# Optimization experiments

Measured on AMD Instinct MI355X. Metric: run time of the kernel, lower is better.

Reference implementation:

```python
import jax, jax.numpy as jnp
import numpy as np

DIM = 128
IND_DIM = 5
HEADS = 4
DIM_HEAD = 32
HIDDEN = HEADS * DIM_HEAD  # 128
SCALE = DIM_HEAD ** -0.5


def setup_inputs() -> dict:
    key = jax.random.key(0)
    ks = jax.random.split(key, 6)
    b, n = 1, 512
    x = jax.random.normal(ks[0], (b, DIM, n), dtype=jnp.float32)
    indicator = jax.random.normal(ks[1], (b, IND_DIM, n, n), dtype=jnp.float32)
    # conv1d kernels with kernel_size=1 are just (out, in) matrices
    w_qkv = jax.random.normal(ks[2], (HIDDEN * 3, DIM), dtype=jnp.float32) * (DIM ** -0.5)
    w_ind = jax.random.normal(ks[3], (HIDDEN * 2, IND_DIM), dtype=jnp.float32) * (IND_DIM ** -0.5)
    w_out = jax.random.normal(ks[4], (DIM, HIDDEN), dtype=jnp.float32) * (HIDDEN ** -0.5)
    b_out = jax.random.normal(ks[5], (DIM,), dtype=jnp.float32) * 0.01
    return {"x": x, "indicator": indicator, "w_qkv": w_qkv,
            "w_ind": w_ind, "w_out": w_out, "b_out": b_out}


def reference(x, indicator, w_qkv, w_ind, w_out, b_out):
    b, c, n = x.shape
    h, dh = HEADS, DIM_HEAD
    # pointwise conv = channel matmul
    qkv = jnp.einsum('oc,bcn->bon', w_qkv, x)  # (b, 3*hidden, n)
    q, k, v = jnp.split(qkv, 3, axis=1)
    q = q.reshape(b, h, dh, n)
    k = k.reshape(b, h, dh, n)
    v = v.reshape(b, h, dh, n)
    ind = jnp.einsum('oc,bcij->boij', w_ind, indicator)  # (b, 2*hidden, n, n)
    ind_q, ind_k = jnp.split(ind, 2, axis=1)
    ind_q = ind_q.reshape(b, h, dh, n, n)
    ind_k = ind_k.reshape(b, h, dh, n, n)
    qq = (q[..., :, None] + ind_q) * SCALE        # (b, h, dh, n, n)
    kk = k[..., None, :] + ind_k                   # (b, h, dh, n, n)
    sim = jnp.einsum('bhdij,bhdij->bhij', qq, kk)  # (b, h, n, n)
    attn = jax.nn.softmax(sim, axis=-1)
    out = jnp.einsum('bhij,bhdj->bhdi', attn, v)   # (b, h, dh, n)
    out = out.reshape(b, h * dh, n)
    return jnp.einsum('oc,bcn->bon', w_out, out) + b_out[None, :, None]
```

## Files before the change

kernel.cpp:

```cpp
#include <hip/hip_runtime.h>
#include <hip/hip_fp16.h>
#include <math.h>

#define N      512
#define DIMC   128
#define HEADS  4
#define DH     32
#define INDC   5
#define SCALE  0.1767766952966369f

#define QKV_ROWS 384
#define AQ_BASE  384
#define AK_BASE  404
#define TOT_ROWS 424
#define NROW_BLK (TOT_ROWS / 4)

#define MHS_F    (TOT_ROWS * N / 2)
#define WOUTT_F  (MHS_F + 128)
#define ATT_F    (WOUTT_F + DIMC * DIMC)

__global__ __launch_bounds__(256) void pre_kernel(const float* __restrict__ w_qkv,
                                                  const float* __restrict__ w_ind,
                                                  const float* __restrict__ x,
                                                  const float* __restrict__ w_out,
                                                  float* __restrict__ ws) {
    const int bx = blockIdx.x;
    const int t  = threadIdx.x;
    __half* rows  = (__half*)ws;
    float* MhS    = ws + MHS_F;
    float* w_outT = ws + WOUTT_F;

    if (bx == NROW_BLK) {
        if (blockIdx.y != 0) return;
        if (t < HEADS * INDC * INDC) {
            const int h = t / 25, idx = t % 25, c = idx / 5, cc = idx % 5;
            float acc = 0.f;
            for (int d = 0; d < DH; ++d)
                acc = fmaf(w_ind[(h * DH + d) * INDC + c],
                           w_ind[(DIMC + h * DH + d) * INDC + cc], acc);
            MhS[h * 32 + idx] = acc;
        }
        for (int idx = t; idx < DIMC * DIMC; idx += 256) {
            const int o = idx >> 7, c = idx & 127;
            w_outT[c * DIMC + o] = w_out[idx];
        }
        return;
    }

    __shared__ float ws2[4 * DIMC];
    const int o0 = bx * 4;
    for (int idx = t; idx < 4 * DIMC; idx += 256) {
        const int r = idx & 3, m = idx >> 2;
        const int row = o0 + r;
        float val;
        if (row < QKV_ROWS) {
            val = w_qkv[row * DIMC + m];
        } else if (row < AK_BASE) {
            const int rr = row - AQ_BASE, h = rr / INDC, c = rr % INDC;
            float acc = 0.f;
            for (int d = 0; d < DH; ++d)
                acc = fmaf(w_qkv[(h * DH + d) * DIMC + m],
                           w_ind[(DIMC + h * DH + d) * INDC + c], acc);
            val = acc;
        } else {
            const int rr = row - AK_BASE, h = rr / INDC, c = rr % INDC;
            float acc = 0.f;
            for (int d = 0; d < DH; ++d)
                acc = fmaf(w_qkv[(DIMC + h * DH + d) * DIMC + m],
                           w_ind[(h * DH + d) * INDC + c], acc);
            val = acc;
        }
        ws2[m * 4 + r] = val;
    }
    __syncthreads();

    const int i = blockIdx.y * 256 + t;
    float acc[4] = {0.f, 0.f, 0.f, 0.f};
#pragma unroll 8
    for (int c = 0; c < DIMC; ++c) {
        const float xv = x[c * N + i];
        const float4 wv = *(const float4*)(ws2 + c * 4);
        acc[0] = fmaf(wv.x, xv, acc[0]);
        acc[1] = fmaf(wv.y, xv, acc[1]);
        acc[2] = fmaf(wv.z, xv, acc[2]);
        acc[3] = fmaf(wv.w, xv, acc[3]);
    }
#pragma unroll
    for (int r = 0; r < 4; ++r) rows[(o0 + r) * N + i] = __float2half(acc[r]);
}

__global__ __launch_bounds__(256) void attn_kernel(const float* __restrict__ ws_c,
                                                   const float* __restrict__ ind,
                                                   float* __restrict__ ws_w) {
    const int t    = threadIdx.x;
    const int lane = t & 63;
    const int wv   = t >> 6;
    const int i    = blockIdx.x * 4 + wv;
    const int h    = blockIdx.y;

    const __half* rows = (const __half*)ws_c;
    const float*  Mh   = ws_c + MHS_F;
    float*        att  = ws_w + ATT_F;

    __shared__ float psh[4][N];

    const __half* q  = rows;
    const __half* Aq = rows + 3 * DIMC * N;
    const float qreg = __half2float(q[(h * DH + (lane & 31)) * N + i]);
    float aq[INDC];
#pragma unroll
    for (int c = 0; c < INDC; ++c)
        aq[c] = __half2float(Aq[(h * INDC + c) * N + i]);
    float M[INDC * INDC];
#pragma unroll
    for (int p = 0; p < INDC * INDC; ++p) M[p] = Mh[h * 32 + p];

    float ic[INDC][8];
#pragma unroll
    for (int c = 0; c < INDC; ++c) {
        const float4* ip = (const float4*)(ind + (c * N + i) * N);
        *(float4*)&ic[c][0] = ip[lane * 2];
        *(float4*)&ic[c][4] = ip[lane * 2 + 1];
    }

    float s[8] = {0.f, 0.f, 0.f, 0.f, 0.f, 0.f, 0.f, 0.f};
    const float4* k4 = (const float4*)(rows + DIMC * N);
#pragma unroll
    for (int d = 0; d < DH; ++d) {
        const float qd = __shfl(qreg, d, 64);
        const float4 kv = k4[(h * DH + d) * 64 + lane];
        const __half2* kh = (const __half2*)&kv;
#pragma unroll
        for (int p = 0; p < 4; ++p) {
            const float2 kf = __half22float2(kh[p]);
            s[p * 2 + 0] = fmaf(qd, kf.x, s[p * 2 + 0]);
            s[p * 2 + 1] = fmaf(qd, kf.y, s[p * 2 + 1]);
        }
    }
    const float4* ak4 = (const float4*)(rows + (3 * DIMC + HEADS * INDC) * N);
#pragma unroll
    for (int c = 0; c < INDC; ++c) {
        const float4 av = ak4[(h * INDC + c) * 64 + lane];
        const __half2* ah = (const __half2*)&av;
#pragma unroll
        for (int p = 0; p < 4; ++p) {
            const float2 af = __half22float2(ah[p]);
            s[p * 2 + 0] = fmaf(aq[c] + af.x, ic[c][p * 2 + 0], s[p * 2 + 0]);
            s[p * 2 + 1] = fmaf(aq[c] + af.y, ic[c][p * 2 + 1], s[p * 2 + 1]);
        }
    }
#pragma unroll
    for (int j = 0; j < 8; ++j) {
        float acc = 0.f;
#pragma unroll
        for (int c = 0; c < INDC; ++c) {
            float tc = 0.f;
#pragma unroll
            for (int cc = 0; cc < INDC; ++cc)
                tc = fmaf(M[c * INDC + cc], ic[cc][j], tc);
            acc = fmaf(ic[c][j], tc, acc);
        }
        s[j] = SCALE * (s[j] + acc);
    }

    float m = s[0];
#pragma unroll
    for (int j = 1; j < 8; ++j) m = fmaxf(m, s[j]);
#pragma unroll
    for (int off = 32; off; off >>= 1) m = fmaxf(m, __shfl_xor(m, off, 64));
    float e[8], sum = 0.f;
#pragma unroll
    for (int j = 0; j < 8; ++j) { e[j] = __expf(s[j] - m); sum += e[j]; }
#pragma unroll
    for (int off = 32; off; off >>= 1) sum += __shfl_xor(sum, off, 64);
    const float rs = 1.f / sum;
#pragma unroll
    for (int j = 0; j < 8; ++j) e[j] *= rs;

    *(float4*)&psh[wv][lane * 8]     = make_float4(e[0], e[1], e[2], e[3]);
    *(float4*)&psh[wv][lane * 8 + 4] = make_float4(e[4], e[5], e[6], e[7]);

    const int d = lane & 31, half = lane >> 5;
    const float4* v4 = (const float4*)(rows + 2 * DIMC * N);
    const float4* pf = (const float4*)&psh[wv][0];
    float acc = 0.f;
#pragma unroll
    for (int kk = 0; kk < 32; ++kk) {
        const float4 vv = v4[(h * DH + d) * 64 + half * 32 + kk];
        const float4 p0 = pf[half * 64 + kk * 2];
        const float4 p1 = pf[half * 64 + kk * 2 + 1];
        const __half2* vh = (const __half2*)&vv;
        const float2 f0 = __half22float2(vh[0]);
        const float2 f1 = __half22float2(vh[1]);
        const float2 f2 = __half22float2(vh[2]);
        const float2 f3 = __half22float2(vh[3]);
        acc = fmaf(p0.x, f0.x, acc); acc = fmaf(p0.y, f0.y, acc);
        acc = fmaf(p0.z, f1.x, acc); acc = fmaf(p0.w, f1.y, acc);
        acc = fmaf(p1.x, f2.x, acc); acc = fmaf(p1.y, f2.y, acc);
        acc = fmaf(p1.z, f3.x, acc); acc = fmaf(p1.w, f3.y, acc);
    }
    acc += __shfl_xor(acc, 32, 64);
    if (lane < 32) att[i * DIMC + h * DH + lane] = acc;
}

__global__ __launch_bounds__(128) void outproj_kernel(const float* __restrict__ ws,
                                                      const float* __restrict__ b_out,
                                                      float* __restrict__ out) {
    const int i = blockIdx.x;
    const int t = threadIdx.x;
    const float* w_outT = ws + WOUTT_F;
    const float* att    = ws + ATT_F;
    __shared__ float av[DIMC];
    av[t] = att[i * DIMC + t];
    __syncthreads();
    float acc = 0.f;
#pragma unroll 8
    for (int c = 0; c < DIMC; ++c)
        acc = fmaf(w_outT[c * DIMC + t], av[c], acc);
    out[t * N + i] = acc + b_out[t];
}

extern "C" void kernel_launch(void* const* d_in, const int* in_sizes, int n_in,
                              void* d_out, int out_size, void* d_ws, size_t ws_size,
                              hipStream_t stream) {
    const float* x         = (const float*)d_in[0];
    const float* indicator = (const float*)d_in[1];
    const float* w_qkv     = (const float*)d_in[2];
    const float* w_ind     = (const float*)d_in[3];
    const float* w_out     = (const float*)d_in[4];
    const float* b_out     = (const float*)d_in[5];
    float* out = (float*)d_out;
    float* ws  = (float*)d_ws;

    pre_kernel<<<dim3(NROW_BLK + 1, 2), 256, 0, stream>>>(w_qkv, w_ind, x, w_out, ws);
    attn_kernel<<<dim3(N / 4, HEADS), 256, 0, stream>>>(ws, indicator, ws);
    outproj_kernel<<<N, 128, 0, stream>>>(ws, b_out, out);
}
```

Measured before the change: 101.6 us.

## Fuse output projection into attention kernel with one query row per block

Each attention block now handles a single query row across all four heads, one wavefront per head, instead of four query rows for one head. The per-row attention output stays in shared memory and the output projection plus bias runs in the same block, split into two halves of the channel sum. This drops the separate outproj launch and the workspace round trip for the attention output. In exchange, each block now loads the indicator slice for its row once per head wavefront, and the grid shape and work per block change.

```diff
diff --git a/kernel.cpp b/kernel.cpp
--- a/kernel.cpp
+++ b/kernel.cpp
@@ -17,7 +17,6 @@
 
 #define MHS_F    (TOT_ROWS * N / 2)
 #define WOUTT_F  (MHS_F + 128)
-#define ATT_F    (WOUTT_F + DIMC * DIMC)
 
 __global__ __launch_bounds__(256) void pre_kernel(const float* __restrict__ w_qkv,
                                                   const float* __restrict__ w_ind,
@@ -91,18 +90,20 @@
 
 __global__ __launch_bounds__(256) void attn_kernel(const float* __restrict__ ws_c,
                                                    const float* __restrict__ ind,
-                                                   float* __restrict__ ws_w) {
+                                                   const float* __restrict__ b_out,
+                                                   float* __restrict__ out) {
     const int t    = threadIdx.x;
     const int lane = t & 63;
-    const int wv   = t >> 6;
-    const int i    = blockIdx.x * 4 + wv;
-    const int h    = blockIdx.y;
-
-    const __half* rows = (const __half*)ws_c;
-    const float*  Mh   = ws_c + MHS_F;
-    float*        att  = ws_w + ATT_F;
-
-    __shared__ float psh[4][N];
+    const int h    = t >> 6;
+    const int i    = blockIdx.x;
+
+    const __half* rows   = (const __half*)ws_c;
+    const float*  Mh     = ws_c + MHS_F;
+    const float*  w_outT = ws_c + WOUTT_F;
+
+    __shared__ float psh[HEADS][N];
+    __shared__ float attv[DIMC];
+    __shared__ float outp[2][DIMC];
 
     const __half* q  = rows;
     const __half* Aq = rows + 3 * DIMC * N;
@@ -177,47 +178,45 @@
 #pragma unroll
     for (int j = 0; j < 8; ++j) e[j] *= rs;
 
-    *(float4*)&psh[wv][lane * 8]     = make_float4(e[0], e[1], e[2], e[3]);
-    *(float4*)&psh[wv][lane * 8 + 4] = make_float4(e[4], e[5], e[6], e[7]);
-
-    const int d = lane & 31, half = lane >> 5;
-    const float4* v4 = (const float4*)(rows + 2 * DIMC * N);
-    const float4* pf = (const float4*)&psh[wv][0];
-    float acc = 0.f;
-#pragma unroll
-    for (int kk = 0; kk < 32; ++kk) {
-        const float4 vv = v4[(h * DH + d) * 64 + half * 32 + kk];
-        const float4 p0 = pf[half * 64 + kk * 2];
-        const float4 p1 = pf[half * 64 + kk * 2 + 1];
-        const __half2* vh = (const __half2*)&vv;
-        const float2 f0 = __half22float2(vh[0]);
-        const float2 f1 = __half22float2(vh[1]);
-        const float2 f2 = __half22float2(vh[2]);
-        const float2 f3 = __half22float2(vh[3]);
-        acc = fmaf(p0.x, f0.x, acc); acc = fmaf(p0.y, f0.y, acc);
-        acc = fmaf(p0.z, f1.x, acc); acc = fmaf(p0.w, f1.y, acc);
-        acc = fmaf(p1.x, f2.x, acc); acc = fmaf(p1.y, f2.y, acc);
-        acc = fmaf(p1.z, f3.x, acc); acc = fmaf(p1.w, f3.y, acc);
-    }
-    acc += __shfl_xor(acc, 32, 64);
-    if (lane < 32) att[i * DIMC + h * DH + lane] = acc;
-}
-
-__global__ __launch_bounds__(128) void outproj_kernel(const float* __restrict__ ws,
-                                                      const float* __restrict__ b_out,
-                                                      float* __restrict__ out) {
-    const int i = blockIdx.x;
-    const int t = threadIdx.x;
-    const float* w_outT = ws + WOUTT_F;
-    const float* att    = ws + ATT_F;
-    __shared__ float av[DIMC];
-    av[t] = att[i * DIMC + t];
+    *(float4*)&psh[h][lane * 8]     = make_float4(e[0], e[1], e[2], e[3]);
+    *(float4*)&psh[h][lane * 8 + 4] = make_float4(e[4], e[5], e[6], e[7]);
+
+    {
+        const int d = lane & 31, half = lane >> 5;
+        const float4* v4 = (const float4*)(rows + 2 * DIMC * N);
+        const float4* pf = (const float4*)&psh[h][0];
+        float acc = 0.f;
+#pragma unroll
+        for (int kk = 0; kk < 32; ++kk) {
+            const float4 vv = v4[(h * DH + d) * 64 + half * 32 + kk];
+            const float4 p0 = pf[half * 64 + kk * 2];
+            const float4 p1 = pf[half * 64 + kk * 2 + 1];
+            const __half2* vh = (const __half2*)&vv;
+            const float2 f0 = __half22float2(vh[0]);
+            const float2 f1 = __half22float2(vh[1]);
+            const float2 f2 = __half22float2(vh[2]);
+            const float2 f3 = __half22float2(vh[3]);
+            acc = fmaf(p0.x, f0.x, acc); acc = fmaf(p0.y, f0.y, acc);
+            acc = fmaf(p0.z, f1.x, acc); acc = fmaf(p0.w, f1.y, acc);
+            acc = fmaf(p1.x, f2.x, acc); acc = fmaf(p1.y, f2.y, acc);
+            acc = fmaf(p1.z, f3.x, acc); acc = fmaf(p1.w, f3.y, acc);
+        }
+        acc += __shfl_xor(acc, 32, 64);
+        if (lane < 32) attv[h * DH + d] = acc;
+    }
     __syncthreads();
-    float acc = 0.f;
+
+    {
+        const int o = t & 127, phase = t >> 7;
+        float acc = 0.f;
 #pragma unroll 8
-    for (int c = 0; c < DIMC; ++c)
-        acc = fmaf(w_outT[c * DIMC + t], av[c], acc);
-    out[t * N + i] = acc + b_out[t];
+        for (int c = phase * 64; c < phase * 64 + 64; ++c)
+            acc = fmaf(w_outT[c * DIMC + o], attv[c], acc);
+        outp[phase][o] = acc;
+    }
+    __syncthreads();
+    if (t < DIMC)
+        out[t * N + i] = outp[0][t] + outp[1][t] + b_out[t];
 }
 
 extern "C" void kernel_launch(void* const* d_in, const int* in_sizes, int n_in,
@@ -233,6 +232,5 @@
     float* ws  = (float*)d_ws;
 
     pre_kernel<<<dim3(NROW_BLK + 1, 2), 256, 0, stream>>>(w_qkv, w_ind, x, w_out, ws);
-    attn_kernel<<<dim3(N / 4, HEADS), 256, 0, stream>>>(ws, indicator, ws);
-    outproj_kernel<<<N, 128, 0, stream>>>(ws, b_out, out);
+    attn_kernel<<<N, 256, 0, stream>>>(ws, indicator, b_out, out);
 }
```

Result: no change. 101.7 us (+0.2%).
